# Kernel tuning notes

Measured on AMD Instinct MI355X. Metric: run time of the kernel, lower is better.

The kernel has to match this reference:

```python
import jax, jax.numpy as jnp
import numpy as np

N = 4096
D = 256
THRESH = 0.04  # default threshold arg of MultiLayerGCN.forward


def setup_inputs() -> dict:
    key = jax.random.key(0)
    ks = jax.random.split(key, 6)
    A = jax.random.normal(ks[0], (N, N), dtype=jnp.float32)
    features = jax.random.normal(ks[1], (N, D), dtype=jnp.float32)
    s = 0.02
    W1 = jax.random.normal(ks[2], (D, D), dtype=jnp.float32) * s
    b1 = jax.random.normal(ks[3], (D,), dtype=jnp.float32) * s
    W2 = jax.random.normal(ks[4], (D, D), dtype=jnp.float32) * s
    b2 = jax.random.normal(ks[5], (D,), dtype=jnp.float32) * s
    return {"A": A, "features": features, "W1": W1, "b1": b1, "W2": W2, "b2": b2}


def _graph_conv(C, out_isqrt, in_isqrt, h, W, b):
    # DGL GraphConv, norm='both': scale src by out_deg^-1/2, aggregate over
    # edges u->v (rst[v] = sum_u C[u,v] * h[u]), scale dst by in_deg^-1/2.
    h = (h * out_isqrt[:, None]) @ W            # [N, out]
    agg = jnp.einsum('uv,ud->vd', C, h)          # C^T @ h, honoring edge direction
    return agg * in_isqrt[:, None] + b


def reference(A, features, W1, b1, W2, b2):
    dt = features.dtype
    mask = (A >= THRESH).astype(dt)
    # add_edges(nodes, nodes) adds self loops on top of surviving diagonal -> counts
    C = mask + jnp.eye(A.shape[0], dtype=dt)
    out_deg = jnp.maximum(C.sum(axis=1), 1.0)    # clamp(min=1) as in DGL
    in_deg = jnp.maximum(C.sum(axis=0), 1.0)
    out_isqrt = jax.lax.rsqrt(out_deg)
    in_isqrt = jax.lax.rsqrt(in_deg)
    h1 = jax.nn.relu(_graph_conv(C, out_isqrt, in_isqrt, features, W1, b1))
    h2 = jax.nn.relu(_graph_conv(C, out_isqrt, in_isqrt, h1, W2, b2))
    return (h1, h2)
```

## Files before the change

### kernel.cpp

```cpp
#include <hip/hip_runtime.h>
#include <stdint.h>

#define NN 4096
#define DD 256
#define TH 0.04f

typedef __attribute__((ext_vector_type(4))) float f32x4;
typedef __attribute__((ext_vector_type(16))) float f32x16;
typedef __attribute__((ext_vector_type(8))) short s16x8;
typedef unsigned short us;

__device__ __forceinline__ us f2bf(float f) {
  union { float f; uint32_t u; } x; x.f = f;
  uint32_t u = x.u;
  return (us)((u + 0x7FFFu + ((u >> 16) & 1u)) >> 16);
}
__device__ __forceinline__ float bf2f(us h) {
  union { uint32_t u; float f; } x; x.u = ((uint32_t)h) << 16;
  return x.f;
}

__device__ __forceinline__ void hw_selfstage(const float* __restrict__ H,
                                             const float* __restrict__ W,
                                             int u0,
                                             us* __restrict__ hWb,
                                             us* __restrict__ hWbP,
                                             char* smem) {
  us (*hs)[264] = reinterpret_cast<us(*)[264]>(smem);
  us (*wt)[34]  = reinterpret_cast<us(*)[34]>(smem + 16 * 264 * 2);
  us (*lt)[260] = reinterpret_cast<us(*)[260]>(smem + 16 * 264 * 2 + 256 * 34 * 2);
  const int t = threadIdx.x;
#pragma unroll
  for (int rep = 0; rep < 4; ++rep) {
    const int flat = rep * 256 + t;
    const int row = flat >> 6, c4 = (flat & 63) * 4;
    f32x4 v = *reinterpret_cast<const f32x4*>(H + (size_t)(u0 + row) * DD + c4);
    uint2 pw;
    pw.x = (uint32_t)f2bf(v[0]) | ((uint32_t)f2bf(v[1]) << 16);
    pw.y = (uint32_t)f2bf(v[2]) | ((uint32_t)f2bf(v[3]) << 16);
    *reinterpret_cast<uint2*>(&hs[row][c4]) = pw;
  }
  const int lane = t & 63, w = t >> 6, l15 = lane & 15, l4 = lane >> 4;
  const f32x4 z = {0.f, 0.f, 0.f, 0.f};
  f32x4 acc[4];
#pragma unroll
  for (int jn = 0; jn < 4; ++jn) acc[jn] = z;
#pragma unroll 1
  for (int ks = 0; ks < 8; ++ks) {
    __syncthreads();
#pragma unroll
    for (int rr = 0; rr < 8; ++rr) {
      const int flat = rr * 256 + t;
      const int k = flat >> 6, d0 = (flat & 63) * 4;
      f32x4 wv = *reinterpret_cast<const f32x4*>(W + (size_t)(ks * 32 + k) * DD + d0);
      wt[d0 + 0][k] = f2bf(wv[0]);
      wt[d0 + 1][k] = f2bf(wv[1]);
      wt[d0 + 2][k] = f2bf(wv[2]);
      wt[d0 + 3][k] = f2bf(wv[3]);
    }
    __syncthreads();
    s16x8 af = *reinterpret_cast<const s16x8*>(&hs[l15][ks * 32 + l4 * 8]);
#pragma unroll
    for (int jn = 0; jn < 4; ++jn) {
      const int dt = w * 4 + jn;
      s16x8 bf = *reinterpret_cast<const s16x8*>(&wt[dt * 16 + l15][l4 * 8]);
      acc[jn] = __builtin_amdgcn_mfma_f32_16x16x32_bf16(af, bf, acc[jn], 0, 0, 0);
    }
  }
#pragma unroll
  for (int jn = 0; jn < 4; ++jn) {
    const int d = w * 64 + jn * 16 + l15;
#pragma unroll
    for (int r = 0; r < 4; ++r) {
      const int ul = l4 * 4 + r;
      us hv = f2bf(acc[jn][r]);
      hWb[(size_t)(u0 + ul) * DD + d] = hv;
      lt[ul][d] = hv;
    }
  }
  __syncthreads();
  const int sg = u0 >> 4;
#pragma unroll
  for (int cc = 0; cc < 2; ++cc) {
    const int c = t * 2 + cc;
    const int dt = c >> 6, lc = c & 63;
    const int ub = (lc >> 5) * 8;
    const int d = dt * 32 + (lc & 31);
    uint4 val;
    val.x = (uint32_t)lt[ub + 0][d] | ((uint32_t)lt[ub + 1][d] << 16);
    val.y = (uint32_t)lt[ub + 2][d] | ((uint32_t)lt[ub + 3][d] << 16);
    val.z = (uint32_t)lt[ub + 4][d] | ((uint32_t)lt[ub + 5][d] << 16);
    val.w = (uint32_t)lt[ub + 6][d] | ((uint32_t)lt[ub + 7][d] << 16);
    *reinterpret_cast<uint4*>(hWbP + ((size_t)dt * 256 + sg) * 512 + lc * 8) = val;
  }
}

__global__ __launch_bounds__(256) void k_scanhw1(const float* __restrict__ A,
                                                 const float* __restrict__ feat,
                                                 const float* __restrict__ W1,
                                                 const float* __restrict__ W2,
                                                 us* __restrict__ bitsT,
                                                 unsigned char* __restrict__ colpart,
                                                 float* __restrict__ oif,
                                                 us* __restrict__ oib,
                                                 us* __restrict__ hWb,
                                                 us* __restrict__ hWbP,
                                                 us* __restrict__ W2TbP) {
  __shared__ __align__(16) char smem[34176];
  if (blockIdx.x >= 512) {
    hw_selfstage(feat, W1, (blockIdx.x - 512) * 16, hWb, hWbP, smem);
    return;
  }
  us* lds16 = reinterpret_cast<us*>(smem);
  const int t = threadIdx.x, b = blockIdx.x;
  const int u0 = b * 8;
  uint32_t cs[16];
#pragma unroll
  for (int k = 0; k < 16; ++k) cs[k] = 0;
#pragma unroll
  for (int rb = 0; rb < 2; ++rb) {
    f32x4 a[4][4];
#pragma unroll
    for (int r = 0; r < 4; ++r) {
      const f32x4* p = reinterpret_cast<const f32x4*>(A + (size_t)(u0 + rb * 4 + r) * NN + t * 16);
#pragma unroll
      for (int c = 0; c < 4; ++c) a[r][c] = p[c];
    }
#pragma unroll
    for (int r = 0; r < 4; ++r) {
      uint32_t m = 0;
#pragma unroll
      for (int c = 0; c < 4; ++c)
#pragma unroll
        for (int j = 0; j < 4; ++j) m |= (a[r][c][j] >= TH ? 1u : 0u) << (c * 4 + j);
      lds16[t * 8 + rb * 4 + r] = (us)m;
#pragma unroll
      for (int k = 0; k < 16; ++k) cs[k] += (m >> k) & 1u;
    }
  }
  uint4 pk;
  pk.x = cs[0]  | (cs[1]  << 8) | (cs[2]  << 16) | (cs[3]  << 24);
  pk.y = cs[4]  | (cs[5]  << 8) | (cs[6]  << 16) | (cs[7]  << 24);
  pk.z = cs[8]  | (cs[9]  << 8) | (cs[10] << 16) | (cs[11] << 24);
  pk.w = cs[12] | (cs[13] << 8) | (cs[14] << 16) | (cs[15] << 24);
  *reinterpret_cast<uint4*>(colpart + (size_t)b * 4096 + t * 16) = pk;
  __syncthreads();
  uint4 wv4 = *reinterpret_cast<const uint4*>(&lds16[t * 8]);
  *reinterpret_cast<uint4*>(bitsT + (size_t)t * 4096 + u0) = wv4;
  if (t < 64) {
    const int r = t >> 3, part = t & 7;
    uint32_t s = 0;
#pragma unroll
    for (int wv = part * 32; wv < part * 32 + 32; ++wv)
      s += (uint32_t)__popc((uint32_t)lds16[wv * 8 + r]);
    s += __shfl_down(s, 4, 8);
    s += __shfl_down(s, 2, 8);
    s += __shfl_down(s, 1, 8);
    if (part == 0) {
      float val = rsqrtf((float)(s + 1u));
      oif[u0 + r] = val;
      oib[u0 + r] = f2bf(val);
    }
  }
  if (b < 16) {
    const int base = b * 4096 + t * 16;
#pragma unroll
    for (int e = 0; e < 16; ++e) {
      const int idx = base + e;
      const int frag = idx >> 9, pos = idx & 511;
      const int lc = pos >> 3, j = pos & 7;
      const int dt = frag >> 3, ks = frag & 7;
      const int k = ks * 32 + (lc >> 4) * 8 + j;
      const int d = dt * 16 + (lc & 15);
      W2TbP[idx] = f2bf(W2[k * 256 + d]);
    }
  }
}

__global__ __launch_bounds__(256) void k_hw2(const float* __restrict__ H,
                                             const us* __restrict__ WP,
                                             us* __restrict__ hWb,
                                             us* __restrict__ hWbP) {
  __shared__ us hs[16][264];
  __shared__ us lt[16][260];
  const int t = threadIdx.x;
  const int u0 = blockIdx.x * 16;
#pragma unroll
  for (int rep = 0; rep < 4; ++rep) {
    const int flat = rep * 256 + t;
    const int row = flat >> 6, c4 = (flat & 63) * 4;
    f32x4 v = *reinterpret_cast<const f32x4*>(H + (size_t)(u0 + row) * DD + c4);
    uint2 pw;
    pw.x = (uint32_t)f2bf(v[0]) | ((uint32_t)f2bf(v[1]) << 16);
    pw.y = (uint32_t)f2bf(v[2]) | ((uint32_t)f2bf(v[3]) << 16);
    *reinterpret_cast<uint2*>(&hs[row][c4]) = pw;
  }
  __syncthreads();
  const int lane = t & 63, w = t >> 6, l15 = lane & 15, l4 = lane >> 4;
  const f32x4 z = {0.f, 0.f, 0.f, 0.f};
  f32x4 acc[4];
#pragma unroll
  for (int jn = 0; jn < 4; ++jn) acc[jn] = z;
#pragma unroll
  for (int ks = 0; ks < 8; ++ks) {
    s16x8 af = *reinterpret_cast<const s16x8*>(&hs[l15][ks * 32 + l4 * 8]);
#pragma unroll
    for (int jn = 0; jn < 4; ++jn) {
      const int dt = w * 4 + jn;
      s16x8 bf = *reinterpret_cast<const s16x8*>(WP + ((size_t)dt * 8 + ks) * 512 + lane * 8);
      acc[jn] = __builtin_amdgcn_mfma_f32_16x16x32_bf16(af, bf, acc[jn], 0, 0, 0);
    }
  }
#pragma unroll
  for (int jn = 0; jn < 4; ++jn) {
    const int d = w * 64 + jn * 16 + l15;
#pragma unroll
    for (int r = 0; r < 4; ++r) {
      const int ul = l4 * 4 + r;
      us hv = f2bf(acc[jn][r]);
      hWb[(size_t)(u0 + ul) * DD + d] = hv;
      lt[ul][d] = hv;
    }
  }
  __syncthreads();
  const int sg = u0 >> 4;
#pragma unroll
  for (int cc = 0; cc < 2; ++cc) {
    const int c = t * 2 + cc;
    const int dt = c >> 6, lc = c & 63;
    const int ub = (lc >> 5) * 8;
    const int d = dt * 32 + (lc & 31);
    uint4 val;
    val.x = (uint32_t)lt[ub + 0][d] | ((uint32_t)lt[ub + 1][d] << 16);
    val.y = (uint32_t)lt[ub + 2][d] | ((uint32_t)lt[ub + 3][d] << 16);
    val.z = (uint32_t)lt[ub + 4][d] | ((uint32_t)lt[ub + 5][d] << 16);
    val.w = (uint32_t)lt[ub + 6][d] | ((uint32_t)lt[ub + 7][d] << 16);
    *reinterpret_cast<uint4*>(hWbP + ((size_t)dt * 256 + sg) * 512 + lc * 8) = val;
  }
}

__global__ __launch_bounds__(512, 2) void k_spmm(const us* __restrict__ bitsT,
                                                 const us* __restrict__ hWbP,
                                                 const us* __restrict__ hWb,
                                                 const float* __restrict__ oif,
                                                 const us* __restrict__ oib,
                                                 const unsigned char* __restrict__ colpart,
                                                 float* __restrict__ ii_g,
                                                 const float* __restrict__ bias,
                                                 float* __restrict__ dst,
                                                 int doii) {
  __shared__ float lds[4 * 64 * 68];
  __shared__ float ii_s[64];
  const int t = threadIdx.x, bb = blockIdx.x;
  const int lane = t & 63, w = t >> 6;
  const int mi = w & 1, kc = w >> 1;
  const int xcd = bb & 7, jj = bb >> 3;
  const int vt = xcd * 8 + (jj >> 2), dq = jj & 3;
  const int V0 = vt * 64, D0 = dq * 64;

  if (doii) {
    uint32_t* sc = reinterpret_cast<uint32_t*>(lds);
    const int v4 = t & 15, c = t >> 4;
    uint32_t s0 = 0, s1 = 0;
#pragma unroll 4
    for (int r = 0; r < 16; ++r) {
      uint32_t x = *reinterpret_cast<const uint32_t*>(colpart + (size_t)(c * 16 + r) * 4096 + V0 + v4 * 4);
      s0 += x & 0x00FF00FFu;
      s1 += (x >> 8) & 0x00FF00FFu;
    }
    sc[(c * 16 + v4) * 2] = s0;
    sc[(c * 16 + v4) * 2 + 1] = s1;
    __syncthreads();
    if (t < 64) {
      const int v4b = t >> 2, sub = t & 3;
      const int reg = sub & 1, hi = sub >> 1;
      uint32_t s = 0;
#pragma unroll
      for (int cc = 0; cc < 32; ++cc)
        s += (sc[(cc * 16 + v4b) * 2 + reg] >> (hi * 16)) & 0xFFFFu;
      float val = rsqrtf((float)(s + 1u));
      ii_s[t] = val;
      ii_g[V0 + t] = val;
    }
    __syncthreads();
  } else {
    if (t < 64) ii_s[t] = ii_g[V0 + t];
    __syncthreads();
  }

  const int l31 = lane & 31, l5 = lane >> 5;
  const uint32_t sh = lane & 15;
  const int wvl = vt * 4 + mi * 2 + ((lane >> 4) & 1);
  const us* Ab = bitsT + (size_t)wvl * 4096 + kc * 1024 + l5 * 8;
  const us* Ob = oib + kc * 1024 + l5 * 8;
  const us* Bp0 = hWbP + ((size_t)(dq * 2 + 0) * 256 + kc * 64) * 512 + lane * 8;
  const us* Bp1 = hWbP + ((size_t)(dq * 2 + 1) * 256 + kc * 64) * 512 + lane * 8;

  f32x16 acc0, acc1;
#pragma unroll
  for (int q = 0; q < 16; ++q) { acc0[q] = 0.f; acc1[q] = 0.f; }

  uint4 h[4]; s16x8 o[4], p0[4], p1[4];
#pragma unroll
  for (int sl = 0; sl < 4; ++sl) {
    h[sl]  = *reinterpret_cast<const uint4*>(Ab + sl * 16);
    o[sl]  = *reinterpret_cast<const s16x8*>(Ob + sl * 16);
    p0[sl] = *reinterpret_cast<const s16x8*>(Bp0 + (size_t)sl * 512);
    p1[sl] = *reinterpret_cast<const s16x8*>(Bp1 + (size_t)sl * 512);
  }

#pragma unroll 1
  for (int it = 0; it < 16; ++it) {
#pragma unroll
    for (int sl = 0; sl < 4; ++sl) {
      union { s16x8 v; uint32_t u[4]; } af;
      const uint32_t* ou = reinterpret_cast<const uint32_t*>(&o[sl]);
      uint32_t m;
      m = ((h[sl].x >> sh) & 0x10001u) * 0xFFFFu; af.u[0] = ou[0] & m;
      m = ((h[sl].y >> sh) & 0x10001u) * 0xFFFFu; af.u[1] = ou[1] & m;
      m = ((h[sl].z >> sh) & 0x10001u) * 0xFFFFu; af.u[2] = ou[2] & m;
      m = ((h[sl].w >> sh) & 0x10001u) * 0xFFFFu; af.u[3] = ou[3] & m;
      acc0 = __builtin_amdgcn_mfma_f32_32x32x16_bf16(af.v, p0[sl], acc0, 0, 0, 0);
      acc1 = __builtin_amdgcn_mfma_f32_32x32x16_bf16(af.v, p1[sl], acc1, 0, 0, 0);
      const int ns = (it * 4 + sl + 4) & 63;
      h[sl]  = *reinterpret_cast<const uint4*>(Ab + ns * 16);
      o[sl]  = *reinterpret_cast<const s16x8*>(Ob + ns * 16);
      p0[sl] = *reinterpret_cast<const s16x8*>(Bp0 + (size_t)ns * 512);
      p1[sl] = *reinterpret_cast<const s16x8*>(Bp1 + (size_t)ns * 512);
    }
  }

  float* buf = lds + (size_t)kc * (64 * 68);
#pragma unroll
  for (int reg = 0; reg < 16; ++reg) {
    const int row = (reg & 3) + 8 * (reg >> 2) + 4 * l5;
    buf[(mi * 32 + row) * 68 + l31] = acc0[reg];
    buf[(mi * 32 + row) * 68 + 32 + l31] = acc1[reg];
  }
  __syncthreads();

  const int vloc = t >> 3, d8 = (t & 7) * 8;
  const int v = V0 + vloc;
  const float* base = lds + vloc * 68 + d8;
  f32x4 s0v = *reinterpret_cast<const f32x4*>(base);
  f32x4 s1v = *reinterpret_cast<const f32x4*>(base + 4);
#pragma unroll
  for (int q = 1; q < 4; ++q) {
    s0v += *reinterpret_cast<const f32x4*>(base + q * (64 * 68));
    s1v += *reinterpret_cast<const f32x4*>(base + q * (64 * 68) + 4);
  }
  union { s16x8 v; us u[8]; } self;
  self.v = *reinterpret_cast<const s16x8*>(hWb + (size_t)v * DD + D0 + d8);
  const float iv = ii_s[vloc];
  const float ov = oif[v];
  const f32x4 bi0 = *reinterpret_cast<const f32x4*>(bias + D0 + d8);
  const f32x4 bi1 = *reinterpret_cast<const f32x4*>(bias + D0 + d8 + 4);
  f32x4 o0, o1;
#pragma unroll
  for (int e = 0; e < 4; ++e) {
    o0[e] = fmaxf((s0v[e] + ov * bf2f(self.u[e])) * iv + bi0[e], 0.f);
    o1[e] = fmaxf((s1v[e] + ov * bf2f(self.u[e + 4])) * iv + bi1[e], 0.f);
  }
  f32x4* po = reinterpret_cast<f32x4*>(dst + (size_t)v * DD + D0 + d8);
  po[0] = o0; po[1] = o1;
}

extern "C" void kernel_launch(void* const* d_in, const int* in_sizes, int n_in,
                              void* d_out, int out_size, void* d_ws, size_t ws_size,
                              hipStream_t stream) {
  const float* A    = (const float*)d_in[0];
  const float* feat = (const float*)d_in[1];
  const float* W1   = (const float*)d_in[2];
  const float* b1   = (const float*)d_in[3];
  const float* W2   = (const float*)d_in[4];
  const float* b2   = (const float*)d_in[5];
  float* out = (float*)d_out;
  char* ws = (char*)d_ws;

  us*            bitsT   = (us*)ws;
  unsigned char* colpart = (unsigned char*)(ws + (2u << 20));
  us*            hWbP    = (us*)(ws + (4u << 20));
  us*            hWb     = (us*)(ws + (6u << 20));
  us*            W2TbP   = (us*)(ws + (8u << 20));
  float*         oif     = (float*)(ws + (8u << 20) + (1u << 17));
  us*            oib     = (us*)(ws + (8u << 20) + (1u << 17) + (16u << 10));
  float*         ii_g    = (float*)(ws + (8u << 20) + (1u << 17) + (24u << 10));

  k_scanhw1<<<768, 256, 0, stream>>>(A, feat, W1, W2, bitsT, colpart, oif, oib,
                                     hWb, hWbP, W2TbP);
  k_spmm<<<256, 512, 0, stream>>>(bitsT, hWbP, hWb, oif, oib, colpart, ii_g, b1, out, 1);
  k_hw2<<<256, 256, 0, stream>>>(out, W2TbP, hWb, hWbP);
  k_spmm<<<256, 512, 0, stream>>>(bitsT, hWbP, hWb, oif, oib, colpart, ii_g, b2,
                                  out + (size_t)NN * DD, 0);
}
```

Baseline: 79.97 us.

## Fuse spmm1, hw2 and spmm2 into one persistent kernel with atomic flags

Replaces three launches (layer-1 SpMM, the layer-2 feature transform, layer-2 SpMM) with a single 640-block kernel. Blocks sync through global atomic counters: hw2 blocks wait on per-row-tile completion counts and spmm2 blocks wait for all hw2 blocks. It also interleaves the scan and hw1 blocks in the first kernel by blockIdx modulo 3, and double-buffers the hW arrays so layer 2 does not overwrite data layer 1 still reads. The aim is to remove launch gaps and kernel-boundary drains. It risks deadlock if waiting blocks are resident before their producers, and adds spin-wait overhead.

Result: slower. 140.3 us (+75.4%).

```diff
diff --git a/kernel.cpp b/kernel.cpp
--- a/kernel.cpp
+++ b/kernel.cpp
@@ -103,17 +103,21 @@
                                                  unsigned char* __restrict__ colpart,
                                                  float* __restrict__ oif,
                                                  us* __restrict__ oib,
-                                                 us* __restrict__ hWb,
-                                                 us* __restrict__ hWbP,
-                                                 us* __restrict__ W2TbP) {
+                                                 us* __restrict__ hWb1,
+                                                 us* __restrict__ hWbP1,
+                                                 us* __restrict__ W2TbP,
+                                                 unsigned int* __restrict__ flags) {
   __shared__ __align__(16) char smem[34176];
-  if (blockIdx.x >= 512) {
-    hw_selfstage(feat, W1, (blockIdx.x - 512) * 16, hWb, hWbP, smem);
+  const int b = blockIdx.x, t = threadIdx.x;
+  const int r3 = b % 3;
+  if (r3 == 2) {
+    hw_selfstage(feat, W1, (b / 3) * 16, hWb1, hWbP1, smem);
     return;
   }
+  const int sb = (b / 3) * 2 + r3;
+  if (b == 0 && t < 72) flags[t] = 0;
   us* lds16 = reinterpret_cast<us*>(smem);
-  const int t = threadIdx.x, b = blockIdx.x;
-  const int u0 = b * 8;
+  const int u0 = sb * 8;
   uint32_t cs[16];
 #pragma unroll
   for (int k = 0; k < 16; ++k) cs[k] = 0;
@@ -143,7 +147,7 @@
   pk.y = cs[4]  | (cs[5]  << 8) | (cs[6]  << 16) | (cs[7]  << 24);
   pk.z = cs[8]  | (cs[9]  << 8) | (cs[10] << 16) | (cs[11] << 24);
   pk.w = cs[12] | (cs[13] << 8) | (cs[14] << 16) | (cs[15] << 24);
-  *reinterpret_cast<uint4*>(colpart + (size_t)b * 4096 + t * 16) = pk;
+  *reinterpret_cast<uint4*>(colpart + (size_t)sb * 4096 + t * 16) = pk;
   __syncthreads();
   uint4 wv4 = *reinterpret_cast<const uint4*>(&lds16[t * 8]);
   *reinterpret_cast<uint4*>(bitsT + (size_t)t * 4096 + u0) = wv4;
@@ -162,8 +166,8 @@
       oib[u0 + r] = f2bf(val);
     }
   }
-  if (b < 16) {
-    const int base = b * 4096 + t * 16;
+  if (sb < 16) {
+    const int base = sb * 4096 + t * 16;
 #pragma unroll
     for (int e = 0; e < 16; ++e) {
       const int idx = base + e;
@@ -177,26 +181,154 @@
   }
 }
 
-__global__ __launch_bounds__(256) void k_hw2(const float* __restrict__ H,
-                                             const us* __restrict__ WP,
-                                             us* __restrict__ hWb,
-                                             us* __restrict__ hWbP) {
-  __shared__ us hs[16][264];
-  __shared__ us lt[16][260];
+__device__ __forceinline__ void spmm_body(const us* __restrict__ bitsT,
+                                          const us* __restrict__ hWbP,
+                                          const us* __restrict__ hWb,
+                                          const float* __restrict__ oif,
+                                          const us* __restrict__ oib,
+                                          const unsigned char* __restrict__ colpart,
+                                          float* __restrict__ ii_g,
+                                          const float* __restrict__ bias,
+                                          float* __restrict__ dst,
+                                          int doii, int bq,
+                                          float* lds, float* ii_s) {
   const int t = threadIdx.x;
-  const int u0 = blockIdx.x * 16;
+  const int lane = t & 63, w = t >> 6;
+  const int mi = w & 1, kc = w >> 1;
+  const int xcd = bq & 7, jj = bq >> 3;
+  const int vt = xcd * 8 + (jj >> 2), dq = jj & 3;
+  const int V0 = vt * 64, D0 = dq * 64;
+
+  if (doii) {
+    uint32_t* sc = reinterpret_cast<uint32_t*>(lds);
+    const int v4 = t & 15, c = t >> 4;
+    uint32_t s0 = 0, s1 = 0;
+#pragma unroll 4
+    for (int r = 0; r < 16; ++r) {
+      uint32_t x = *reinterpret_cast<const uint32_t*>(colpart + (size_t)(c * 16 + r) * 4096 + V0 + v4 * 4);
+      s0 += x & 0x00FF00FFu;
+      s1 += (x >> 8) & 0x00FF00FFu;
+    }
+    sc[(c * 16 + v4) * 2] = s0;
+    sc[(c * 16 + v4) * 2 + 1] = s1;
+    __syncthreads();
+    if (t < 64) {
+      const int v4b = t >> 2, sub = t & 3;
+      const int reg = sub & 1, hi = sub >> 1;
+      uint32_t s = 0;
+#pragma unroll
+      for (int cc = 0; cc < 32; ++cc)
+        s += (sc[(cc * 16 + v4b) * 2 + reg] >> (hi * 16)) & 0xFFFFu;
+      float val = rsqrtf((float)(s + 1u));
+      ii_s[t] = val;
+      ii_g[V0 + t] = val;
+    }
+    __syncthreads();
+  } else {
+    if (t < 64) ii_s[t] = ii_g[V0 + t];
+    __syncthreads();
+  }
+
+  const int l31 = lane & 31, l5 = lane >> 5;
+  const uint32_t sh = lane & 15;
+  const int wvl = vt * 4 + mi * 2 + ((lane >> 4) & 1);
+  const us* Ab = bitsT + (size_t)wvl * 4096 + kc * 1024 + l5 * 8;
+  const us* Ob = oib + kc * 1024 + l5 * 8;
+  const us* Bp0 = hWbP + ((size_t)(dq * 2 + 0) * 256 + kc * 64) * 512 + lane * 8;
+  const us* Bp1 = hWbP + ((size_t)(dq * 2 + 1) * 256 + kc * 64) * 512 + lane * 8;
+
+  f32x16 acc0, acc1;
+#pragma unroll
+  for (int q = 0; q < 16; ++q) { acc0[q] = 0.f; acc1[q] = 0.f; }
+
+  uint4 h[4]; s16x8 o[4], p0[4], p1[4];
+#pragma unroll
+  for (int sl = 0; sl < 4; ++sl) {
+    h[sl]  = *reinterpret_cast<const uint4*>(Ab + sl * 16);
+    o[sl]  = *reinterpret_cast<const s16x8*>(Ob + sl * 16);
+    p0[sl] = *reinterpret_cast<const s16x8*>(Bp0 + (size_t)sl * 512);
+    p1[sl] = *reinterpret_cast<const s16x8*>(Bp1 + (size_t)sl * 512);
+  }
+
+#pragma unroll 1
+  for (int it = 0; it < 16; ++it) {
+#pragma unroll
+    for (int sl = 0; sl < 4; ++sl) {
+      union { s16x8 v; uint32_t u[4]; } af;
+      const uint32_t* ou = reinterpret_cast<const uint32_t*>(&o[sl]);
+      uint32_t m;
+      m = (h[sl].x >> sh) & 0x10001u; af.u[0] = ou[0] & ((m << 16) - m);
+      m = (h[sl].y >> sh) & 0x10001u; af.u[1] = ou[1] & ((m << 16) - m);
+      m = (h[sl].z >> sh) & 0x10001u; af.u[2] = ou[2] & ((m << 16) - m);
+      m = (h[sl].w >> sh) & 0x10001u; af.u[3] = ou[3] & ((m << 16) - m);
+      acc0 = __builtin_amdgcn_mfma_f32_32x32x16_bf16(af.v, p0[sl], acc0, 0, 0, 0);
+      acc1 = __builtin_amdgcn_mfma_f32_32x32x16_bf16(af.v, p1[sl], acc1, 0, 0, 0);
+      const int ns = (it * 4 + sl + 4) & 63;
+      h[sl]  = *reinterpret_cast<const uint4*>(Ab + ns * 16);
+      o[sl]  = *reinterpret_cast<const s16x8*>(Ob + ns * 16);
+      p0[sl] = *reinterpret_cast<const s16x8*>(Bp0 + (size_t)ns * 512);
+      p1[sl] = *reinterpret_cast<const s16x8*>(Bp1 + (size_t)ns * 512);
+    }
+  }
+
+  float* buf = lds + (size_t)kc * (64 * 68);
+#pragma unroll
+  for (int reg = 0; reg < 16; ++reg) {
+    const int row = (reg & 3) + 8 * (reg >> 2) + 4 * l5;
+    buf[(mi * 32 + row) * 68 + l31] = acc0[reg];
+    buf[(mi * 32 + row) * 68 + 32 + l31] = acc1[reg];
+  }
+  __syncthreads();
+
+  const int vloc = t >> 3, d8 = (t & 7) * 8;
+  const int v = V0 + vloc;
+  const float* base = lds + vloc * 68 + d8;
+  f32x4 s0v = *reinterpret_cast<const f32x4*>(base);
+  f32x4 s1v = *reinterpret_cast<const f32x4*>(base + 4);
+#pragma unroll
+  for (int q = 1; q < 4; ++q) {
+    s0v += *reinterpret_cast<const f32x4*>(base + q * (64 * 68));
+    s1v += *reinterpret_cast<const f32x4*>(base + q * (64 * 68) + 4);
+  }
+  union { s16x8 v; us u[8]; } self;
+  self.v = *reinterpret_cast<const s16x8*>(hWb + (size_t)v * DD + D0 + d8);
+  const float iv = ii_s[vloc];
+  const float ov = oif[v];
+  const f32x4 bi0 = *reinterpret_cast<const f32x4*>(bias + D0 + d8);
+  const f32x4 bi1 = *reinterpret_cast<const f32x4*>(bias + D0 + d8 + 4);
+  f32x4 o0, o1;
+#pragma unroll
+  for (int e = 0; e < 4; ++e) {
+    o0[e] = fmaxf((s0v[e] + ov * bf2f(self.u[e])) * iv + bi0[e], 0.f);
+    o1[e] = fmaxf((s1v[e] + ov * bf2f(self.u[e + 4])) * iv + bi1[e], 0.f);
+  }
+  f32x4* po = reinterpret_cast<f32x4*>(dst + (size_t)v * DD + D0 + d8);
+  po[0] = o0; po[1] = o1;
+}
+
+__device__ __forceinline__ void hw2_block(const float* __restrict__ H,
+                                          const us* __restrict__ WP,
+                                          int u0,
+                                          us* __restrict__ hWb,
+                                          us* __restrict__ hWbP,
+                                          char* smem) {
+  const int t = threadIdx.x;
+  const int unit = t >> 8, tt = t & 255;
+  const int su0 = u0 + unit * 16;
+  us (*hs)[264] = reinterpret_cast<us(*)[264]>(smem + unit * 16768);
+  us (*lt)[260] = reinterpret_cast<us(*)[260]>(smem + unit * 16768 + 8448);
 #pragma unroll
   for (int rep = 0; rep < 4; ++rep) {
-    const int flat = rep * 256 + t;
+    const int flat = rep * 256 + tt;
     const int row = flat >> 6, c4 = (flat & 63) * 4;
-    f32x4 v = *reinterpret_cast<const f32x4*>(H + (size_t)(u0 + row) * DD + c4);
+    f32x4 v = *reinterpret_cast<const f32x4*>(H + (size_t)(su0 + row) * DD + c4);
     uint2 pw;
     pw.x = (uint32_t)f2bf(v[0]) | ((uint32_t)f2bf(v[1]) << 16);
     pw.y = (uint32_t)f2bf(v[2]) | ((uint32_t)f2bf(v[3]) << 16);
     *reinterpret_cast<uint2*>(&hs[row][c4]) = pw;
   }
   __syncthreads();
-  const int lane = t & 63, w = t >> 6, l15 = lane & 15, l4 = lane >> 4;
+  const int lane = tt & 63, w4 = tt >> 6, l15 = lane & 15, l4 = lane >> 4;
   const f32x4 z = {0.f, 0.f, 0.f, 0.f};
   f32x4 acc[4];
 #pragma unroll
@@ -206,27 +338,27 @@
     s16x8 af = *reinterpret_cast<const s16x8*>(&hs[l15][ks * 32 + l4 * 8]);
 #pragma unroll
     for (int jn = 0; jn < 4; ++jn) {
-      const int dt = w * 4 + jn;
+      const int dt = w4 * 4 + jn;
       s16x8 bf = *reinterpret_cast<const s16x8*>(WP + ((size_t)dt * 8 + ks) * 512 + lane * 8);
       acc[jn] = __builtin_amdgcn_mfma_f32_16x16x32_bf16(af, bf, acc[jn], 0, 0, 0);
     }
   }
 #pragma unroll
   for (int jn = 0; jn < 4; ++jn) {
-    const int d = w * 64 + jn * 16 + l15;
+    const int d = w4 * 64 + jn * 16 + l15;
 #pragma unroll
     for (int r = 0; r < 4; ++r) {
       const int ul = l4 * 4 + r;
       us hv = f2bf(acc[jn][r]);
-      hWb[(size_t)(u0 + ul) * DD + d] = hv;
+      hWb[(size_t)(su0 + ul) * DD + d] = hv;
       lt[ul][d] = hv;
     }
   }
   __syncthreads();
-  const int sg = u0 >> 4;
+  const int sg = su0 >> 4;
 #pragma unroll
   for (int cc = 0; cc < 2; ++cc) {
-    const int c = t * 2 + cc;
+    const int c = tt * 2 + cc;
     const int dt = c >> 6, lc = c & 63;
     const int ub = (lc >> 5) * 8;
     const int d = dt * 32 + (lc & 31);
@@ -239,130 +371,58 @@
   }
 }
 
-__global__ __launch_bounds__(512, 2) void k_spmm(const us* __restrict__ bitsT,
-                                                 const us* __restrict__ hWbP,
-                                                 const us* __restrict__ hWb,
+__global__ __launch_bounds__(512, 2) void k_mega(const us* __restrict__ bitsT,
+                                                 const us* __restrict__ hWbP1,
+                                                 const us* __restrict__ hWb1,
+                                                 us* __restrict__ hWbP2,
+                                                 us* __restrict__ hWb2,
+                                                 const us* __restrict__ W2TbP,
                                                  const float* __restrict__ oif,
                                                  const us* __restrict__ oib,
                                                  const unsigned char* __restrict__ colpart,
                                                  float* __restrict__ ii_g,
-                                                 const float* __restrict__ bias,
-                                                 float* __restrict__ dst,
-                                                 int doii) {
-  __shared__ float lds[4 * 64 * 68];
-  __shared__ float ii_s[64];
+                                                 const float* __restrict__ b1,
+                                                 const float* __restrict__ b2,
+                                                 float* __restrict__ out,
+                                                 unsigned int* __restrict__ flags) {
+  __shared__ __align__(16) float lds[4 * 64 * 68 + 64];
   const int t = threadIdx.x, bb = blockIdx.x;
-  const int lane = t & 63, w = t >> 6;
-  const int mi = w & 1, kc = w >> 1;
-  const int xcd = bb & 7, jj = bb >> 3;
-  const int vt = xcd * 8 + (jj >> 2), dq = jj & 3;
-  const int V0 = vt * 64, D0 = dq * 64;
-
-  if (doii) {
-    uint32_t* sc = reinterpret_cast<uint32_t*>(lds);
-    const int v4 = t & 15, c = t >> 4;
-    uint32_t s0 = 0, s1 = 0;
-#pragma unroll 4
-    for (int r = 0; r < 16; ++r) {
-      uint32_t x = *reinterpret_cast<const uint32_t*>(colpart + (size_t)(c * 16 + r) * 4096 + V0 + v4 * 4);
-      s0 += x & 0x00FF00FFu;
-      s1 += (x >> 8) & 0x00FF00FFu;
-    }
-    sc[(c * 16 + v4) * 2] = s0;
-    sc[(c * 16 + v4) * 2 + 1] = s1;
-    __syncthreads();
-    if (t < 64) {
-      const int v4b = t >> 2, sub = t & 3;
-      const int reg = sub & 1, hi = sub >> 1;
-      uint32_t s = 0;
-#pragma unroll
-      for (int cc = 0; cc < 32; ++cc)
-        s += (sc[(cc * 16 + v4b) * 2 + reg] >> (hi * 16)) & 0xFFFFu;
-      float val = rsqrtf((float)(s + 1u));
-      ii_s[t] = val;
-      ii_g[V0 + t] = val;
-    }
-    __syncthreads();
+  unsigned int* cnt_vt = flags;
+  unsigned int* done2 = flags + 64;
+
+  if (bb < 256) {
+    spmm_body(bitsT, hWbP1, hWb1, oif, oib, colpart, ii_g, b1, out, 1, bb,
+              lds, lds + 4 * 64 * 68);
+    __syncthreads();
+    if (t == 0) {
+      const int vt = (bb & 7) * 8 + ((bb >> 3) >> 2);
+      __threadfence();
+      __hip_atomic_fetch_add(&cnt_vt[vt], 1u, __ATOMIC_RELEASE, __HIP_MEMORY_SCOPE_AGENT);
+    }
+  } else if (bb < 384) {
+    const int u0 = (bb - 256) * 32;
+    if (t == 0) {
+      while (__hip_atomic_load(&cnt_vt[u0 >> 6], __ATOMIC_ACQUIRE, __HIP_MEMORY_SCOPE_AGENT) < 4u)
+        __builtin_amdgcn_s_sleep(8);
+      __threadfence();
+    }
+    __syncthreads();
+    hw2_block(out, W2TbP, u0, hWb2, hWbP2, reinterpret_cast<char*>(lds));
+    __syncthreads();
+    if (t == 0) {
+      __threadfence();
+      __hip_atomic_fetch_add(done2, 1u, __ATOMIC_RELEASE, __HIP_MEMORY_SCOPE_AGENT);
+    }
   } else {
-    if (t < 64) ii_s[t] = ii_g[V0 + t];
-    __syncthreads();
-  }
-
-  const int l31 = lane & 31, l5 = lane >> 5;
-  const uint32_t sh = lane & 15;
-  const int wvl = vt * 4 + mi * 2 + ((lane >> 4) & 1);
-  const us* Ab = bitsT + (size_t)wvl * 4096 + kc * 1024 + l5 * 8;
-  const us* Ob = oib + kc * 1024 + l5 * 8;
-  const us* Bp0 = hWbP + ((size_t)(dq * 2 + 0) * 256 + kc * 64) * 512 + lane * 8;
-  const us* Bp1 = hWbP + ((size_t)(dq * 2 + 1) * 256 + kc * 64) * 512 + lane * 8;
-
-  f32x16 acc0, acc1;
-#pragma unroll
-  for (int q = 0; q < 16; ++q) { acc0[q] = 0.f; acc1[q] = 0.f; }
-
-  uint4 h[4]; s16x8 o[4], p0[4], p1[4];
-#pragma unroll
-  for (int sl = 0; sl < 4; ++sl) {
-    h[sl]  = *reinterpret_cast<const uint4*>(Ab + sl * 16);
-    o[sl]  = *reinterpret_cast<const s16x8*>(Ob + sl * 16);
-    p0[sl] = *reinterpret_cast<const s16x8*>(Bp0 + (size_t)sl * 512);
-    p1[sl] = *reinterpret_cast<const s16x8*>(Bp1 + (size_t)sl * 512);
-  }
-
-#pragma unroll 1
-  for (int it = 0; it < 16; ++it) {
-#pragma unroll
-    for (int sl = 0; sl < 4; ++sl) {
-      union { s16x8 v; uint32_t u[4]; } af;
-      const uint32_t* ou = reinterpret_cast<const uint32_t*>(&o[sl]);
-      uint32_t m;
-      m = ((h[sl].x >> sh) & 0x10001u) * 0xFFFFu; af.u[0] = ou[0] & m;
-      m = ((h[sl].y >> sh) & 0x10001u) * 0xFFFFu; af.u[1] = ou[1] & m;
-      m = ((h[sl].z >> sh) & 0x10001u) * 0xFFFFu; af.u[2] = ou[2] & m;
-      m = ((h[sl].w >> sh) & 0x10001u) * 0xFFFFu; af.u[3] = ou[3] & m;
-      acc0 = __builtin_amdgcn_mfma_f32_32x32x16_bf16(af.v, p0[sl], acc0, 0, 0, 0);
-      acc1 = __builtin_amdgcn_mfma_f32_32x32x16_bf16(af.v, p1[sl], acc1, 0, 0, 0);
-      const int ns = (it * 4 + sl + 4) & 63;
-      h[sl]  = *reinterpret_cast<const uint4*>(Ab + ns * 16);
-      o[sl]  = *reinterpret_cast<const s16x8*>(Ob + ns * 16);
-      p0[sl] = *reinterpret_cast<const s16x8*>(Bp0 + (size_t)ns * 512);
-      p1[sl] = *reinterpret_cast<const s16x8*>(Bp1 + (size_t)ns * 512);
-    }
-  }
-
-  float* buf = lds + (size_t)kc * (64 * 68);
-#pragma unroll
-  for (int reg = 0; reg < 16; ++reg) {
-    const int row = (reg & 3) + 8 * (reg >> 2) + 4 * l5;
-    buf[(mi * 32 + row) * 68 + l31] = acc0[reg];
-    buf[(mi * 32 + row) * 68 + 32 + l31] = acc1[reg];
-  }
-  __syncthreads();
-
-  const int vloc = t >> 3, d8 = (t & 7) * 8;
-  const int v = V0 + vloc;
-  const float* base = lds + vloc * 68 + d8;
-  f32x4 s0v = *reinterpret_cast<const f32x4*>(base);
-  f32x4 s1v = *reinterpret_cast<const f32x4*>(base + 4);
-#pragma unroll
-  for (int q = 1; q < 4; ++q) {
-    s0v += *reinterpret_cast<const f32x4*>(base + q * (64 * 68));
-    s1v += *reinterpret_cast<const f32x4*>(base + q * (64 * 68) + 4);
-  }
-  union { s16x8 v; us u[8]; } self;
-  self.v = *reinterpret_cast<const s16x8*>(hWb + (size_t)v * DD + D0 + d8);
-  const float iv = ii_s[vloc];
-  const float ov = oif[v];
-  const f32x4 bi0 = *reinterpret_cast<const f32x4*>(bias + D0 + d8);
-  const f32x4 bi1 = *reinterpret_cast<const f32x4*>(bias + D0 + d8 + 4);
-  f32x4 o0, o1;
-#pragma unroll
-  for (int e = 0; e < 4; ++e) {
-    o0[e] = fmaxf((s0v[e] + ov * bf2f(self.u[e])) * iv + bi0[e], 0.f);
-    o1[e] = fmaxf((s1v[e] + ov * bf2f(self.u[e + 4])) * iv + bi1[e], 0.f);
-  }
-  f32x4* po = reinterpret_cast<f32x4*>(dst + (size_t)v * DD + D0 + d8);
-  po[0] = o0; po[1] = o1;
+    if (t == 0) {
+      while (__hip_atomic_load(done2, __ATOMIC_ACQUIRE, __HIP_MEMORY_SCOPE_AGENT) < 128u)
+        __builtin_amdgcn_s_sleep(8);
+      __threadfence();
+    }
+    __syncthreads();
+    spmm_body(bitsT, hWbP2, hWb2, oif, oib, colpart, ii_g, b2,
+              out + (size_t)NN * DD, 0, bb - 384, lds, lds + 4 * 64 * 68);
+  }
 }
 
 extern "C" void kernel_launch(void* const* d_in, const int* in_sizes, int n_in,
@@ -379,17 +439,18 @@
 
   us*            bitsT   = (us*)ws;
   unsigned char* colpart = (unsigned char*)(ws + (2u << 20));
-  us*            hWbP    = (us*)(ws + (4u << 20));
-  us*            hWb     = (us*)(ws + (6u << 20));
-  us*            W2TbP   = (us*)(ws + (8u << 20));
-  float*         oif     = (float*)(ws + (8u << 20) + (1u << 17));
-  us*            oib     = (us*)(ws + (8u << 20) + (1u << 17) + (16u << 10));
-  float*         ii_g    = (float*)(ws + (8u << 20) + (1u << 17) + (24u << 10));
+  us*            hWbP1   = (us*)(ws + (4u << 20));
+  us*            hWb1    = (us*)(ws + (6u << 20));
+  us*            hWbP2   = (us*)(ws + (8u << 20));
+  us*            hWb2    = (us*)(ws + (10u << 20));
+  us*            W2TbP   = (us*)(ws + (12u << 20));
+  float*         oif     = (float*)(ws + (12u << 20) + (1u << 17));
+  us*            oib     = (us*)(ws + (12u << 20) + (1u << 17) + (16u << 10));
+  float*         ii_g    = (float*)(ws + (12u << 20) + (1u << 17) + (24u << 10));
+  unsigned int*  flags   = (unsigned int*)(ws + (12u << 20) + (1u << 17) + (40u << 10));
 
   k_scanhw1<<<768, 256, 0, stream>>>(A, feat, W1, W2, bitsT, colpart, oif, oib,
-                                     hWb, hWbP, W2TbP);
-  k_spmm<<<256, 512, 0, stream>>>(bitsT, hWbP, hWb, oif, oib, colpart, ii_g, b1, out, 1);
-  k_hw2<<<256, 256, 0, stream>>>(out, W2TbP, hWb, hWbP);
-  k_spmm<<<256, 512, 0, stream>>>(bitsT, hWbP, hWb, oif, oib, colpart, ii_g, b2,
-                                  out + (size_t)NN * DD, 0);
-}
+                                     hWb1, hWbP1, W2TbP, flags);
+  k_mega<<<640, 512, 0, stream>>>(bitsT, hWbP1, hWb1, hWbP2, hWb2, W2TbP,
+                                  oif, oib, colpart, ii_g, b1, b2, out, flags);
+}
```

## Template spmm per layer, fold out-degree scale into hW2, interleave scan blocks

Applied to the files above, without the earlier changes.

The spmm kernel becomes a template on the layer. The main MFMA loop now runs before the in-degree reduction in layer 1, and layer 2 skips loading the out-degree vector because k_hw2 now pre-multiplies hW by out_isqrt. The layer-2 A operand is built directly as bf16 1.0 from the mask bits. The scan kernel interleaves hW1 blocks with scan blocks (every third block) so the two kinds of work share the GPU concurrently. Layer 2 also gets separate hW buffers, which uses more workspace.

New measurement: 70.94 us. 1.13x faster.

```diff
diff --git a/kernel.cpp b/kernel.cpp
--- a/kernel.cpp
+++ b/kernel.cpp
@@ -103,17 +103,19 @@
                                                  unsigned char* __restrict__ colpart,
                                                  float* __restrict__ oif,
                                                  us* __restrict__ oib,
-                                                 us* __restrict__ hWb,
-                                                 us* __restrict__ hWbP,
+                                                 us* __restrict__ hWb1,
+                                                 us* __restrict__ hWbP1,
                                                  us* __restrict__ W2TbP) {
   __shared__ __align__(16) char smem[34176];
-  if (blockIdx.x >= 512) {
-    hw_selfstage(feat, W1, (blockIdx.x - 512) * 16, hWb, hWbP, smem);
+  const int b = blockIdx.x, t = threadIdx.x;
+  const int r3 = b % 3;
+  if (r3 == 2) {
+    hw_selfstage(feat, W1, (b / 3) * 16, hWb1, hWbP1, smem);
     return;
   }
+  const int sb = (b / 3) * 2 + r3;
   us* lds16 = reinterpret_cast<us*>(smem);
-  const int t = threadIdx.x, b = blockIdx.x;
-  const int u0 = b * 8;
+  const int u0 = sb * 8;
   uint32_t cs[16];
 #pragma unroll
   for (int k = 0; k < 16; ++k) cs[k] = 0;
@@ -143,7 +145,7 @@
   pk.y = cs[4]  | (cs[5]  << 8) | (cs[6]  << 16) | (cs[7]  << 24);
   pk.z = cs[8]  | (cs[9]  << 8) | (cs[10] << 16) | (cs[11] << 24);
   pk.w = cs[12] | (cs[13] << 8) | (cs[14] << 16) | (cs[15] << 24);
-  *reinterpret_cast<uint4*>(colpart + (size_t)b * 4096 + t * 16) = pk;
+  *reinterpret_cast<uint4*>(colpart + (size_t)sb * 4096 + t * 16) = pk;
   __syncthreads();
   uint4 wv4 = *reinterpret_cast<const uint4*>(&lds16[t * 8]);
   *reinterpret_cast<uint4*>(bitsT + (size_t)t * 4096 + u0) = wv4;
@@ -162,8 +164,8 @@
       oib[u0 + r] = f2bf(val);
     }
   }
-  if (b < 16) {
-    const int base = b * 4096 + t * 16;
+  if (sb < 16) {
+    const int base = sb * 4096 + t * 16;
 #pragma unroll
     for (int e = 0; e < 16; ++e) {
       const int idx = base + e;
@@ -179,6 +181,7 @@
 
 __global__ __launch_bounds__(256) void k_hw2(const float* __restrict__ H,
                                              const us* __restrict__ WP,
+                                             const float* __restrict__ oif,
                                              us* __restrict__ hWb,
                                              us* __restrict__ hWbP) {
   __shared__ us hs[16][264];
@@ -211,13 +214,16 @@
       acc[jn] = __builtin_amdgcn_mfma_f32_16x16x32_bf16(af, bf, acc[jn], 0, 0, 0);
     }
   }
+  float oifv[4];
+#pragma unroll
+  for (int r = 0; r < 4; ++r) oifv[r] = oif[u0 + l4 * 4 + r];
 #pragma unroll
   for (int jn = 0; jn < 4; ++jn) {
     const int d = w * 64 + jn * 16 + l15;
 #pragma unroll
     for (int r = 0; r < 4; ++r) {
       const int ul = l4 * 4 + r;
-      us hv = f2bf(acc[jn][r]);
+      us hv = f2bf(acc[jn][r] * oifv[r]);
       hWb[(size_t)(u0 + ul) * DD + d] = hv;
       lt[ul][d] = hv;
     }
@@ -239,6 +245,7 @@
   }
 }
 
+template <int L1>
 __global__ __launch_bounds__(512, 2) void k_spmm(const us* __restrict__ bitsT,
                                                  const us* __restrict__ hWbP,
                                                  const us* __restrict__ hWb,
@@ -247,18 +254,66 @@
                                                  const unsigned char* __restrict__ colpart,
                                                  float* __restrict__ ii_g,
                                                  const float* __restrict__ bias,
-                                                 float* __restrict__ dst,
-                                                 int doii) {
+                                                 float* __restrict__ dst) {
   __shared__ float lds[4 * 64 * 68];
   __shared__ float ii_s[64];
-  const int t = threadIdx.x, bb = blockIdx.x;
+  const int t = threadIdx.x, bq = blockIdx.x;
   const int lane = t & 63, w = t >> 6;
   const int mi = w & 1, kc = w >> 1;
-  const int xcd = bb & 7, jj = bb >> 3;
+  const int xcd = bq & 7, jj = bq >> 3;
   const int vt = xcd * 8 + (jj >> 2), dq = jj & 3;
   const int V0 = vt * 64, D0 = dq * 64;
 
-  if (doii) {
+  const int l31 = lane & 31, l5 = lane >> 5;
+  const uint32_t sh = lane & 15;
+  const int wvl = vt * 4 + mi * 2 + ((lane >> 4) & 1);
+  const us* Ab = bitsT + (size_t)wvl * 4096 + kc * 1024 + l5 * 8;
+  const us* Ob = oib + kc * 1024 + l5 * 8;
+  const us* Bp0 = hWbP + ((size_t)(dq * 2 + 0) * 256 + kc * 64) * 512 + lane * 8;
+  const us* Bp1 = hWbP + ((size_t)(dq * 2 + 1) * 256 + kc * 64) * 512 + lane * 8;
+
+  f32x16 acc0, acc1;
+#pragma unroll
+  for (int q = 0; q < 16; ++q) { acc0[q] = 0.f; acc1[q] = 0.f; }
+
+  uint4 h[4]; s16x8 o[4], p0[4], p1[4];
+#pragma unroll
+  for (int sl = 0; sl < 4; ++sl) {
+    h[sl]  = *reinterpret_cast<const uint4*>(Ab + sl * 16);
+    if (L1) o[sl] = *reinterpret_cast<const s16x8*>(Ob + sl * 16);
+    p0[sl] = *reinterpret_cast<const s16x8*>(Bp0 + (size_t)sl * 512);
+    p1[sl] = *reinterpret_cast<const s16x8*>(Bp1 + (size_t)sl * 512);
+  }
+
+#pragma unroll 1
+  for (int it = 0; it < 16; ++it) {
+#pragma unroll
+    for (int sl = 0; sl < 4; ++sl) {
+      union { s16x8 v; uint32_t u[4]; } af;
+      uint32_t m;
+      if (L1) {
+        const uint32_t* ou = reinterpret_cast<const uint32_t*>(&o[sl]);
+        m = (h[sl].x >> sh) & 0x10001u; af.u[0] = ou[0] & ((m << 16) - m);
+        m = (h[sl].y >> sh) & 0x10001u; af.u[1] = ou[1] & ((m << 16) - m);
+        m = (h[sl].z >> sh) & 0x10001u; af.u[2] = ou[2] & ((m << 16) - m);
+        m = (h[sl].w >> sh) & 0x10001u; af.u[3] = ou[3] & ((m << 16) - m);
+      } else {
+        m = (h[sl].x >> sh) & 0x10001u; af.u[0] = m * 0x3F80u;
+        m = (h[sl].y >> sh) & 0x10001u; af.u[1] = m * 0x3F80u;
+        m = (h[sl].z >> sh) & 0x10001u; af.u[2] = m * 0x3F80u;
+        m = (h[sl].w >> sh) & 0x10001u; af.u[3] = m * 0x3F80u;
+      }
+      acc0 = __builtin_amdgcn_mfma_f32_32x32x16_bf16(af.v, p0[sl], acc0, 0, 0, 0);
+      acc1 = __builtin_amdgcn_mfma_f32_32x32x16_bf16(af.v, p1[sl], acc1, 0, 0, 0);
+      const int ns = (it * 4 + sl + 4) & 63;
+      h[sl]  = *reinterpret_cast<const uint4*>(Ab + ns * 16);
+      if (L1) o[sl] = *reinterpret_cast<const s16x8*>(Ob + ns * 16);
+      p0[sl] = *reinterpret_cast<const s16x8*>(Bp0 + (size_t)ns * 512);
+      p1[sl] = *reinterpret_cast<const s16x8*>(Bp1 + (size_t)ns * 512);
+    }
+  }
+
+  if (L1) {
     uint32_t* sc = reinterpret_cast<uint32_t*>(lds);
     const int v4 = t & 15, c = t >> 4;
     uint32_t s0 = 0, s1 = 0;
@@ -285,49 +340,6 @@
     __syncthreads();
   } else {
     if (t < 64) ii_s[t] = ii_g[V0 + t];
-    __syncthreads();
-  }
-
-  const int l31 = lane & 31, l5 = lane >> 5;
-  const uint32_t sh = lane & 15;
-  const int wvl = vt * 4 + mi * 2 + ((lane >> 4) & 1);
-  const us* Ab = bitsT + (size_t)wvl * 4096 + kc * 1024 + l5 * 8;
-  const us* Ob = oib + kc * 1024 + l5 * 8;
-  const us* Bp0 = hWbP + ((size_t)(dq * 2 + 0) * 256 + kc * 64) * 512 + lane * 8;
-  const us* Bp1 = hWbP + ((size_t)(dq * 2 + 1) * 256 + kc * 64) * 512 + lane * 8;
-
-  f32x16 acc0, acc1;
-#pragma unroll
-  for (int q = 0; q < 16; ++q) { acc0[q] = 0.f; acc1[q] = 0.f; }
-
-  uint4 h[4]; s16x8 o[4], p0[4], p1[4];
-#pragma unroll
-  for (int sl = 0; sl < 4; ++sl) {
-    h[sl]  = *reinterpret_cast<const uint4*>(Ab + sl * 16);
-    o[sl]  = *reinterpret_cast<const s16x8*>(Ob + sl * 16);
-    p0[sl] = *reinterpret_cast<const s16x8*>(Bp0 + (size_t)sl * 512);
-    p1[sl] = *reinterpret_cast<const s16x8*>(Bp1 + (size_t)sl * 512);
-  }
-
-#pragma unroll 1
-  for (int it = 0; it < 16; ++it) {
-#pragma unroll
-    for (int sl = 0; sl < 4; ++sl) {
-      union { s16x8 v; uint32_t u[4]; } af;
-      const uint32_t* ou = reinterpret_cast<const uint32_t*>(&o[sl]);
-      uint32_t m;
-      m = ((h[sl].x >> sh) & 0x10001u) * 0xFFFFu; af.u[0] = ou[0] & m;
-      m = ((h[sl].y >> sh) & 0x10001u) * 0xFFFFu; af.u[1] = ou[1] & m;
-      m = ((h[sl].z >> sh) & 0x10001u) * 0xFFFFu; af.u[2] = ou[2] & m;
-      m = ((h[sl].w >> sh) & 0x10001u) * 0xFFFFu; af.u[3] = ou[3] & m;
-      acc0 = __builtin_amdgcn_mfma_f32_32x32x16_bf16(af.v, p0[sl], acc0, 0, 0, 0);
-      acc1 = __builtin_amdgcn_mfma_f32_32x32x16_bf16(af.v, p1[sl], acc1, 0, 0, 0);
-      const int ns = (it * 4 + sl + 4) & 63;
-      h[sl]  = *reinterpret_cast<const uint4*>(Ab + ns * 16);
-      o[sl]  = *reinterpret_cast<const s16x8*>(Ob + ns * 16);
-      p0[sl] = *reinterpret_cast<const s16x8*>(Bp0 + (size_t)ns * 512);
-      p1[sl] = *reinterpret_cast<const s16x8*>(Bp1 + (size_t)ns * 512);
-    }
   }
 
   float* buf = lds + (size_t)kc * (64 * 68);
@@ -352,7 +364,7 @@
   union { s16x8 v; us u[8]; } self;
   self.v = *reinterpret_cast<const s16x8*>(hWb + (size_t)v * DD + D0 + d8);
   const float iv = ii_s[vloc];
-  const float ov = oif[v];
+  const float ov = L1 ? oif[v] : 1.0f;
   const f32x4 bi0 = *reinterpret_cast<const f32x4*>(bias + D0 + d8);
   const f32x4 bi1 = *reinterpret_cast<const f32x4*>(bias + D0 + d8 + 4);
   f32x4 o0, o1;
@@ -379,17 +391,20 @@
 
   us*            bitsT   = (us*)ws;
   unsigned char* colpart = (unsigned char*)(ws + (2u << 20));
-  us*            hWbP    = (us*)(ws + (4u << 20));
-  us*            hWb     = (us*)(ws + (6u << 20));
-  us*            W2TbP   = (us*)(ws + (8u << 20));
-  float*         oif     = (float*)(ws + (8u << 20) + (1u << 17));
-  us*            oib     = (us*)(ws + (8u << 20) + (1u << 17) + (16u << 10));
-  float*         ii_g    = (float*)(ws + (8u << 20) + (1u << 17) + (24u << 10));
+  us*            hWbP1   = (us*)(ws + (4u << 20));
+  us*            hWb1    = (us*)(ws + (6u << 20));
+  us*            hWbP2   = (us*)(ws + (8u << 20));
+  us*            hWb2    = (us*)(ws + (10u << 20));
+  us*            W2TbP   = (us*)(ws + (12u << 20));
+  float*         oif     = (float*)(ws + (12u << 20) + (1u << 17));
+  us*            oib     = (us*)(ws + (12u << 20) + (1u << 17) + (16u << 10));
+  float*         ii_g    = (float*)(ws + (12u << 20) + (1u << 17) + (24u << 10));
 
   k_scanhw1<<<768, 256, 0, stream>>>(A, feat, W1, W2, bitsT, colpart, oif, oib,
-                                     hWb, hWbP, W2TbP);
-  k_spmm<<<256, 512, 0, stream>>>(bitsT, hWbP, hWb, oif, oib, colpart, ii_g, b1, out, 1);
-  k_hw2<<<256, 256, 0, stream>>>(out, W2TbP, hWb, hWbP);
-  k_spmm<<<256, 512, 0, stream>>>(bitsT, hWbP, hWb, oif, oib, colpart, ii_g, b2,
-                                  out + (size_t)NN * DD, 0);
-}
+                                     hWb1, hWbP1, W2TbP);
+  k_spmm<1><<<256, 512, 0, stream>>>(bitsT, hWbP1, hWb1, oif, oib, colpart,
+                                     ii_g, b1, out);
+  k_hw2<<<256, 256, 0, stream>>>(out, W2TbP, oif, hWb2, hWbP2);
+  k_spmm<0><<<256, 512, 0, stream>>>(bitsT, hWbP2, hWb2, oif, oib, colpart,
+                                     ii_g, b2, out + (size_t)NN * DD);
+}
```
